# Kernel optimization log

Measured on AMD Instinct MI355X. Metric: run time of the kernel, lower is better.

The kernel has to match this reference:

```python
import jax, jax.numpy as jnp
import numpy as np

B, N = 4, 1024
D1, D2 = 512, 512
C = 512          # out_c = outdim_self[2] = ln_dim
H = 8            # cross_num_heads
DH = C // H      # head dim
LAYERS = 3       # cross_layer
LN_EPS = 1e-5


def _layer_norm(x, gamma, beta):
    mu = jnp.mean(x, axis=-1, keepdims=True)
    var = jnp.mean(jnp.square(x - mu), axis=-1, keepdims=True)
    return (x - mu) * jax.lax.rsqrt(var + LN_EPS) * gamma + beta


def setup_inputs() -> dict:
    key = jax.random.key(0)
    ks = jax.random.split(key, 5)
    s1, s2, sv = 1.0 / np.sqrt(D1), 1.0 / np.sqrt(D2), 1.0 / np.sqrt(D1 + D2)
    return {
        "x1": jax.random.normal(ks[0], (B, N, D1), jnp.float32),
        "x2": jax.random.normal(ks[1], (B, N, D2), jnp.float32),
        "Wq": jax.random.uniform(ks[2], (C, D1), jnp.float32, -s1, s1),
        "Wk": jax.random.uniform(ks[3], (C, D2), jnp.float32, -s2, s2),
        "Wv": jax.random.uniform(ks[4], (C, D1 + D2), jnp.float32, -sv, sv),
        "ln_gamma": jnp.ones((C,), jnp.float32),
        "ln_beta": jnp.zeros((C,), jnp.float32),
    }


def reference(x1, x2, Wq, Wk, Wv, ln_gamma, ln_beta):
    x = jnp.concatenate((x1, x2), axis=2)                      # [B,N,D1+D2]
    scale = x1.shape[-1] ** (-0.5)                             # uses x1 feature dim
    # [B,N,C] -> [B,H,N,DH]
    to_heads = lambda t: t.reshape(B, N, H, DH).transpose(0, 2, 1, 3)
    Q = to_heads(jnp.einsum('bnd,cd->bnc', x1, Wq))
    K = to_heads(jnp.einsum('bnd,cd->bnc', x2, Wk))
    V = to_heads(jnp.einsum('bnd,cd->bnc', x, Wv))

    output = None
    for _ in range(LAYERS):
        attn = jnp.einsum('bhnd,bhmd->bhnm', Q, K) * scale     # [B,H,N,N]
        mask = attn != 0
        attn = jnp.where(mask, attn, -1e20)
        attn = jax.nn.softmax(attn, axis=-1)
        attn = attn * mask
        V1 = jnp.einsum('bhnm,bhmd->bhnd', attn, V)            # [B,H,N,DH]
        V1 = V1.transpose(0, 2, 1, 3).reshape(B, N, C)
        Vr = V.transpose(0, 2, 1, 3).reshape(B, N, C)
        output = _layer_norm(V1 + Vr, ln_gamma, ln_beta)       # [B,N,C]
        V = to_heads(output)
    return output
```

## Files before the change

### kernel.cpp

```cpp
#include <hip/hip_runtime.h>


#define LOG2E 1.44269504088896f

using f32x4   = __attribute__((ext_vector_type(4))) float;
using short8  = __attribute__((ext_vector_type(8))) short;
using ushort8 = __attribute__((ext_vector_type(8))) unsigned short;
using ushort4v= __attribute__((ext_vector_type(4))) unsigned short;
using uchar8  = __attribute__((ext_vector_type(8))) unsigned char;
using uchar4v = __attribute__((ext_vector_type(4))) unsigned char;
using uchar16 = __attribute__((ext_vector_type(16))) unsigned char;

__device__ inline unsigned short f2bf(float f) {
  unsigned u = __builtin_bit_cast(unsigned, f);
  u += 0x7fffu + ((u >> 16) & 1u);
  return (unsigned short)(u >> 16);
}
__device__ inline float bf2f(unsigned short h) {
  unsigned u = (unsigned)h << 16;
  return __builtin_bit_cast(float, u);
}

__device__ inline unsigned char f2e4m3_fast(float f) {
  unsigned u = __builtin_bit_cast(unsigned, f);
  unsigned sign = (u >> 24) & 0x80u;
  unsigned a = u & 0x7fffffffu;
  unsigned v = a + (0x7ffffu + ((a >> 20) & 1u));
  unsigned m = (v >> 20) - 960u;
  m = (m > 126u) ? 126u : m;
  m = (a < 0x3c000000u) ? 0u : m;
  return (unsigned char)(sign | m);
}

__device__ inline f32x4 mfma_bf16(short8 a, short8 b, f32x4 c) {
  return __builtin_amdgcn_mfma_f32_16x16x32_bf16(a, b, c, 0, 0, 0);
}

__device__ inline void gload_lds16(const void* g, void* l) {
  __builtin_amdgcn_global_load_lds(
      (const __attribute__((address_space(1))) unsigned int*)g,
      (__attribute__((address_space(3))) unsigned int*)l, 16, 0, 0);
}

__device__ inline int swz(int row, int byte_in_row) {
  return row * 128 + (byte_in_row ^ ((row & 7) << 4));
}

__global__ __launch_bounds__(256) void k_convert_all(
    const float* __restrict__ x1, const float* __restrict__ x2,
    const float* __restrict__ Wq, const float* __restrict__ Wk,
    const float* __restrict__ Wv,
    unsigned short* __restrict__ xb, unsigned short* __restrict__ Wqb,
    unsigned short* __restrict__ Wkb, unsigned short* __restrict__ Wvb) {
  int i = blockIdx.x * 256 + threadIdx.x;
  const float* src;
  unsigned short* dst;
  if (i < 524288) {
    int e0 = i * 8, m = e0 >> 10, d = e0 & 1023;
    src = (d < 512) ? (x1 + (size_t)m * 512 + d)
                    : (x2 + (size_t)m * 512 + (d - 512));
    dst = xb + (size_t)e0;
  } else if (i < 557056) {
    int j = (i - 524288) * 8;
    src = Wq + j; dst = Wqb + j;
  } else if (i < 589824) {
    int j = (i - 557056) * 8;
    src = Wk + j; dst = Wkb + j;
  } else {
    int j = (i - 589824) * 8;
    src = Wv + j; dst = Wvb + j;
  }
  float4 a = ((const float4*)src)[0];
  float4 b = ((const float4*)src)[1];
  ushort8 o;
  o[0] = f2bf(a.x); o[1] = f2bf(a.y); o[2] = f2bf(a.z); o[3] = f2bf(a.w);
  o[4] = f2bf(b.x); o[5] = f2bf(b.y); o[6] = f2bf(b.z); o[7] = f2bf(b.w);
  *(ushort8*)dst = o;
}

__global__ __launch_bounds__(256) void k_proj(
    const unsigned short* __restrict__ xb,
    const unsigned short* __restrict__ Wqb,
    const unsigned short* __restrict__ Wkb,
    const unsigned short* __restrict__ Wvb,
    unsigned short* __restrict__ Qb, unsigned short* __restrict__ Kb,
    float* __restrict__ Vf, unsigned char* __restrict__ VtF8, int writeVt) {
  __shared__ __align__(16) unsigned short Atile[128 * 64];
  __shared__ __align__(16) unsigned short Btile[128 * 64];

  const int id  = blockIdx.x;
  const int z   = id % 3;
  const int rem = id / 3;
  const int c0  = (rem & 3) * 128;
  const int m0  = (rem >> 2) * 128;

  const int K    = (z == 2) ? 1024 : 512;
  const int aoff = (z == 1) ? 512 : 0;
  const unsigned short* W = (z == 0) ? Wqb : (z == 1) ? Wkb : Wvb;

  const int t  = threadIdx.x;
  const int w  = t >> 6, l = t & 63;
  const int lr = l & 15, ls = l >> 4;
  const int wr = w >> 1, wc = w & 1;

  const int srow  = l >> 3;
  const int scol8 = (l & 7) * 8;

  f32x4 acc[4][4] = {};

  for (int k0 = 0; k0 < K; k0 += 64) {
#pragma unroll
    for (int j = 0; j < 4; ++j) {
      int ch  = w * 4 + j;
      int row = ch * 8 + srow;
      gload_lds16(xb + (size_t)(m0 + row) * 1024 + aoff + k0 + scol8,
                  Atile + ch * 512);
      gload_lds16(W + (size_t)(c0 + row) * K + k0 + scol8,
                  Btile + ch * 512);
    }
    __syncthreads();
#pragma unroll
    for (int ks = 0; ks < 2; ++ks) {
      short8 af[4], bf[4];
#pragma unroll
      for (int mf = 0; mf < 4; ++mf)
        af[mf] = *(const short8*)(Atile + (wr * 64 + mf * 16 + lr) * 64 +
                                  ks * 32 + ls * 8);
#pragma unroll
      for (int nf = 0; nf < 4; ++nf)
        bf[nf] = *(const short8*)(Btile + (wc * 64 + nf * 16 + lr) * 64 +
                                  ks * 32 + ls * 8);
#pragma unroll
      for (int mf = 0; mf < 4; ++mf)
#pragma unroll
        for (int nf = 0; nf < 4; ++nf)
          acc[mf][nf] = mfma_bf16(af[mf], bf[nf], acc[mf][nf]);
    }
    __syncthreads();
  }

#pragma unroll
  for (int mf = 0; mf < 4; ++mf)
#pragma unroll
    for (int nf = 0; nf < 4; ++nf) {
      int m = m0 + wr * 64 + mf * 16 + ls * 4;
      int c = c0 + wc * 64 + nf * 16 + lr;
      if (z == 2) {
#pragma unroll
        for (int r = 0; r < 4; ++r)
          Vf[(size_t)(m + r) * 512 + c] = acc[mf][nf][r];
        if (writeVt) {
          int b = m >> 10, n = m & 1023, h = c >> 6, dh = c & 63;
          uchar4v o;
#pragma unroll
          for (int r = 0; r < 4; ++r) o[r] = f2e4m3_fast(acc[mf][nf][r]);
          char* dst = (char*)VtF8 +
                      ((size_t)((b * 8 + h) * 64 + dh)) * 1024 + (n & ~127) +
                      ((n & 127) ^ ((dh & 7) << 4));
          *(uchar4v*)dst = o;
        }
      } else {
#pragma unroll
        for (int r = 0; r < 4; ++r) {
          int mm = m + r;
          int b = mm >> 10, n = mm & 1023, h = c >> 6, dh = c & 63;
          size_t idx = ((size_t)(b * 8 + h) * 1024 + n) * 64 + dh;
          (z == 0 ? Qb : Kb)[idx] = f2bf(acc[mf][nf][r]);
        }
      }
    }
}

__global__ __launch_bounds__(256) void k_transpose_v(
    const float* __restrict__ Vf, void* __restrict__ Vt) {
  __shared__ unsigned short tile[64 * 66];
  const int bh = blockIdx.y;
  const int b = bh >> 3, h = bh & 7;
  const int n0 = blockIdx.x * 64;
  const int t = threadIdx.x;
  {
    int n = t >> 2, dh0 = (t & 3) * 16;
    const float* src = Vf + ((size_t)b * 1024 + n0 + n) * 512 + h * 64 + dh0;
    unsigned short* dst = tile + n * 66 + dh0;
#pragma unroll
    for (int j = 0; j < 16; j += 4) {
      float4 v = *(const float4*)(src + j);
      dst[j + 0] = f2bf(v.x); dst[j + 1] = f2bf(v.y);
      dst[j + 2] = f2bf(v.z); dst[j + 3] = f2bf(v.w);
    }
  }
  __syncthreads();
#pragma unroll
  for (int it = 0; it < 2; ++it) {
    int dh = (t >> 3) + it * 32, n8 = (t & 7) * 8;
    ushort8 o;
#pragma unroll
    for (int j = 0; j < 8; ++j) o[j] = tile[(n8 + j) * 66 + dh];
    char* dst = (char*)Vt + ((size_t)(bh * 64 + dh)) * 2048 + n0 * 2 +
                ((n8 * 2) ^ ((dh & 7) << 4));
    *(ushort8*)dst = o;
  }
}

__global__ __launch_bounds__(256) void k_scores(
    const unsigned short* __restrict__ Qb,
    const unsigned short* __restrict__ Kb,
    unsigned char* __restrict__ Pmat, float* __restrict__ lsum_g) {
  __shared__ char lds[2 * 8192 + 4 * 16 * 80];
  char* kbuf0 = lds;
  char* kbuf1 = lds + 8192;
  const int id  = blockIdx.x;
  const int lid = (id & 7) * 256 + (id >> 3);
  const int bh  = lid >> 6;
  const int q0  = ((lid >> 2) & 15) * 64;
  const int kq  = lid & 3;
  const int t = threadIdx.x;
  const int w = t >> 6, l = t & 63, lr = l & 15, ls = l >> 4;
  char* pbuf = lds + 16384 + w * (16 * 80);

  const float sclog2e = 0.0637587160f;

  short8 qa[2];
  {
    const unsigned short* Qg =
        Qb + ((size_t)bh * 1024 + q0 + w * 16 + lr) * 64 + ls * 8;
    qa[0] = *(const short8*)(Qg);
    qa[1] = *(const short8*)(Qg + 32);
  }

  const unsigned short* Kg = Kb + (size_t)bh * 1024 * 64 + kq * 256 * 64;
  unsigned char* Pg = Pmat + (size_t)bh * 1024 * 1024;

  float lacc[4] = {0.f, 0.f, 0.f, 0.f};

  const int srow = t >> 3, sc8 = (t & 7) * 8;
  int4 kreg[2];
  kreg[0] = *(const int4*)(Kg + (size_t)(srow)*64 + sc8);
  kreg[1] = *(const int4*)(Kg + (size_t)(srow + 32) * 64 + sc8);
  {
    char* kb = kbuf0;
    *(int4*)(kb + swz(srow, sc8 * 2)) = kreg[0];
    *(int4*)(kb + swz(srow + 32, sc8 * 2)) = kreg[1];
  }

  for (int kc = 0; kc < 4; ++kc) {
    __syncthreads();
    char* kb  = (kc & 1) ? kbuf1 : kbuf0;
    char* kbn = (kc & 1) ? kbuf0 : kbuf1;
    if (kc < 3) {
      kreg[0] = *(const int4*)(Kg + (size_t)((kc + 1) * 64 + srow) * 64 + sc8);
      kreg[1] = *(const int4*)(Kg + (size_t)((kc + 1) * 64 + srow + 32) * 64 + sc8);
    }

    f32x4 s[4] = {};
#pragma unroll
    for (int kk = 0; kk < 2; ++kk) {
#pragma unroll
      for (int nt = 0; nt < 4; ++nt) {
        short8 bk = *(const short8*)(kb + swz(nt * 16 + lr, kk * 64 + ls * 16));
        s[nt] = mfma_bf16(qa[kk], bk, s[nt]);
      }
    }

#pragma unroll
    for (int nt = 0; nt < 4; ++nt)
#pragma unroll
      for (int r = 0; r < 4; ++r) {
        float sv = s[nt][r];
        float pv = (sv == 0.f) ? 0.f : __builtin_amdgcn_exp2f(sv * sclog2e);
        lacc[r] += pv;
        pbuf[(ls * 4 + r) * 80 + nt * 16 + lr] = (char)f2e4m3_fast(pv);
      }

    int gkc = kq * 4 + kc;
    {
      int prow = l >> 2, pchk = l & 3;
      uchar16 pv16 = *(const uchar16*)(pbuf + prow * 80 + pchk * 16);
      int n = q0 + w * 16 + prow;
      *(uchar16*)(Pg + (size_t)n * 1024 + (gkc >> 1) * 128 +
                  (((gkc & 1) * 64 + pchk * 16) ^ ((n & 7) << 4))) = pv16;
    }

    if (kc < 3) {
      *(int4*)(kbn + swz(srow, sc8 * 2)) = kreg[0];
      *(int4*)(kbn + swz(srow + 32, sc8 * 2)) = kreg[1];
    }
  }

#pragma unroll
  for (int r = 0; r < 4; ++r) {
#pragma unroll
    for (int off = 1; off < 16; off <<= 1)
      lacc[r] += __shfl_xor(lacc[r], off, 64);
  }
  if (lr == 0) {
#pragma unroll
    for (int r = 0; r < 4; ++r)
      lsum_g[kq * 32768 + (size_t)bh * 1024 + q0 + w * 16 + ls * 4 + r] =
          lacc[r];
  }
}

__global__ __launch_bounds__(256) void k_pv(
    const unsigned char* __restrict__ Pmat,
    const unsigned char* __restrict__ Vt,
    const float* __restrict__ lsum_g, unsigned short* __restrict__ V1a,
    unsigned short* __restrict__ V1b) {
  __shared__ __align__(16) char Ab[2][8192];
  __shared__ __align__(16) char Bb[2][8192];
  const int id  = blockIdx.x;
  const int lid = (id & 7) * 128 + (id >> 3);
  const int head = lid >> 5;
  const int n0   = ((lid >> 1) & 15) * 64;
  const int mh   = lid & 1;
  const int t = threadIdx.x;
  const int w = t >> 6, l = t & 63, lr = l & 15, ls = l >> 4;

  const char* Pg = (const char*)(Pmat + (size_t)head * 1024 * 1024) +
                   (size_t)n0 * 1024 + mh * 512;
  const char* Vg = (const char*)(Vt + (size_t)head * 64 * 1024) + mh * 512;

  const int srow = w * 16 + (l >> 3);
  const int sc16 = (l & 7) * 16;

  f32x4 acc[4] = {};

  auto STAGE = [&](int buf, int kc) {
#pragma unroll
    for (int j = 0; j < 2; ++j) {
      int row = srow + j * 8;
      gload_lds16(Pg + (size_t)row * 1024 + kc * 128 + sc16,
                  &Ab[buf][w * 2048 + j * 1024]);
      gload_lds16(Vg + (size_t)row * 1024 + kc * 128 + sc16,
                  &Bb[buf][w * 2048 + j * 1024]);
    }
  };

  STAGE(0, 0);
  __syncthreads();
  int cur = 0;
  for (int kc = 0; kc < 4; ++kc) {
    if (kc < 3) STAGE(cur ^ 1, kc + 1);
#pragma unroll
    for (int ks = 0; ks < 4; ++ks) {
      long af = *(const long*)(&Ab[cur][swz(w * 16 + lr, ks * 32 + ls * 8)]);
#pragma unroll
      for (int nf = 0; nf < 4; ++nf) {
        long bf8 = *(const long*)(&Bb[cur][swz(nf * 16 + lr, ks * 32 + ls * 8)]);
        acc[nf] = __builtin_amdgcn_mfma_f32_16x16x32_fp8_fp8(af, bf8, acc[nf],
                                                             0, 0, 0);
      }
    }
    __syncthreads();
    cur ^= 1;
  }

  unsigned short* V1 = mh ? V1b : V1a;
  const int b = head >> 3, h = head & 7;
#pragma unroll
  for (int r = 0; r < 4; ++r) {
    int n = n0 + w * 16 + ls * 4 + r;
    size_t li = (size_t)head * 1024 + n;
    float lv = lsum_g[li] + lsum_g[32768 + li] + lsum_g[65536 + li] +
               lsum_g[98304 + li];
    float rinv = (lv > 0.f) ? 1.f / lv : 0.f;
#pragma unroll
    for (int nf = 0; nf < 4; ++nf)
      V1[((size_t)b * 1024 + n) * 512 + h * 64 + nf * 16 + lr] =
          f2bf(acc[nf][r] * rinv);
  }
}

__global__ __launch_bounds__(256) void k_ln_t(
    const unsigned short* __restrict__ V1a,
    const unsigned short* __restrict__ V1b,
    const float* __restrict__ Vf_in,
    const float* __restrict__ gamma, const float* __restrict__ beta,
    float* __restrict__ Vf_out, void* __restrict__ Vt, int mode) {
  __shared__ unsigned short tile[4 * 520];
  const int blk = blockIdx.x;
  const int b  = blk >> 8;
  const int n0 = (blk & 255) * 4;
  const int t = threadIdx.x;
  const int row = t >> 6;
  const int l = t & 63;
  const int c0 = l * 8;
  const size_t base = ((size_t)b * 1024 + n0 + row) * 512 + c0;

  float x[8];
  float s = 0.f, sq = 0.f;
  {
    ushort8 a0 = *(const ushort8*)(V1a + base);
    ushort8 a1 = *(const ushort8*)(V1b + base);
    float4 v0 = *(const float4*)(Vf_in + base);
    float4 v1 = *(const float4*)(Vf_in + base + 4);
#pragma unroll
    for (int j = 0; j < 8; ++j) {
      float vf = (j < 4) ? ((const float*)&v0)[j] : ((const float*)&v1)[j - 4];
      float y = bf2f(a0[j]) + bf2f(a1[j]) + vf;
      x[j] = y;
      s += y;
      sq += y * y;
    }
  }
#pragma unroll
  for (int off = 1; off < 64; off <<= 1) {
    s  += __shfl_xor(s, off, 64);
    sq += __shfl_xor(sq, off, 64);
  }
  float mu   = s * (1.f / 512.f);
  float var  = sq * (1.f / 512.f) - mu * mu;
  float rstd = rsqrtf(var + 1e-5f);

  unsigned short* trow = tile + row * 520 + c0;
#pragma unroll
  for (int j = 0; j < 8; j += 4) {
    float4 g = *(const float4*)(gamma + c0 + j);
    float4 bb = *(const float4*)(beta + c0 + j);
    float4 y;
    y.x = (x[j + 0] - mu) * rstd * g.x + bb.x;
    y.y = (x[j + 1] - mu) * rstd * g.y + bb.y;
    y.z = (x[j + 2] - mu) * rstd * g.z + bb.z;
    y.w = (x[j + 3] - mu) * rstd * g.w + bb.w;
    *(float4*)(Vf_out + base + j) = y;
    if (mode != 2) {
      trow[j + 0] = f2bf(y.x); trow[j + 1] = f2bf(y.y);
      trow[j + 2] = f2bf(y.z); trow[j + 3] = f2bf(y.w);
    }
  }
  if (mode == 2) return;
  __syncthreads();

#pragma unroll
  for (int it = 0; it < 2; ++it) {
    int d = t + it * 256;
    int h = d >> 6, dh = d & 63;
    int sw = (dh & 7) << 4;
    if (mode == 0) {
      ushort4v o;
#pragma unroll
      for (int j = 0; j < 4; ++j) o[j] = tile[j * 520 + d];
      int byte0 = n0 * 2;
      char* dst = (char*)Vt + ((size_t)((b * 8 + h) * 64 + dh)) * 2048 +
                  (byte0 & ~127) + ((byte0 & 127) ^ sw);
      *(ushort4v*)dst = o;
    } else {
      uchar4v o;
#pragma unroll
      for (int j = 0; j < 4; ++j) o[j] = f2e4m3_fast(bf2f(tile[j * 520 + d]));
      char* dst = (char*)Vt + ((size_t)((b * 8 + h) * 64 + dh)) * 1024 +
                  (n0 & ~127) + ((n0 & 127) ^ sw);
      *(uchar4v*)dst = o;
    }
  }
}

__global__ __launch_bounds__(256) void k_attn(
    const unsigned short* __restrict__ Qb,
    const unsigned short* __restrict__ Kb,
    const unsigned short* __restrict__ Vt,
    unsigned short* __restrict__ V1) {
  __shared__ char lds[8192 + 8192 + 4 * 16 * 144];
  char* kbuf = lds;
  char* vbuf = lds + 8192;
  const int bh = blockIdx.y;
  const int q0 = blockIdx.x * 64;
  const int t = threadIdx.x;
  const int w = t >> 6, l = t & 63, lr = l & 15, ls = l >> 4;
  char* pbuf = lds + 16384 + w * (16 * 144);

  const float scale = 0.044194173824159216f;

  short8 qa[2];
  {
    const unsigned short* Qg =
        Qb + ((size_t)bh * 1024 + q0 + w * 16 + lr) * 64 + ls * 8;
    qa[0] = *(const short8*)(Qg);
    qa[1] = *(const short8*)(Qg + 32);
  }

  f32x4 O[4] = {};
  float mrow[4], lrow[4];
#pragma unroll
  for (int r = 0; r < 4; ++r) { mrow[r] = -INFINITY; lrow[r] = 0.f; }

  const unsigned short* Kg = Kb + (size_t)bh * 1024 * 64;
  const char* Vg = (const char*)(Vt + (size_t)bh * 64 * 1024);

  for (int kc = 0; kc < 16; ++kc) {
    {
      int row = t >> 3;
      int c8  = (t & 7) * 8;
#pragma unroll
      for (int it = 0; it < 2; ++it) {
        int rr = row + it * 32;
        int4 kv = *(const int4*)(Kg + (size_t)(kc * 64 + rr) * 64 + c8);
        *(int4*)(kbuf + swz(rr, c8 * 2)) = kv;
        int swv = (rr & 7) << 4;
        int4 vv = *(const int4*)(Vg + (size_t)rr * 2048 + kc * 128 +
                                 ((c8 * 2) ^ swv));
        *(int4*)(vbuf + swz(rr, c8 * 2)) = vv;
      }
    }
    __syncthreads();

    f32x4 s[4] = {};
#pragma unroll
    for (int kk = 0; kk < 2; ++kk) {
#pragma unroll
      for (int nt = 0; nt < 4; ++nt) {
        short8 bk = *(const short8*)(kbuf + swz(nt * 16 + lr, kk * 64 + ls * 16));
        s[nt] = mfma_bf16(qa[kk], bk, s[nt]);
      }
    }

    float p[4][4];
    float cmax[4];
#pragma unroll
    for (int r = 0; r < 4; ++r) cmax[r] = -INFINITY;
#pragma unroll
    for (int nt = 0; nt < 4; ++nt)
#pragma unroll
      for (int r = 0; r < 4; ++r) {
        float sv = s[nt][r];
        p[nt][r] = (sv == 0.f) ? -INFINITY : sv * scale;
        cmax[r] = fmaxf(cmax[r], p[nt][r]);
      }
#pragma unroll
    for (int r = 0; r < 4; ++r)
#pragma unroll
      for (int off = 1; off < 16; off <<= 1)
        cmax[r] = fmaxf(cmax[r], __shfl_xor(cmax[r], off, 64));

    float alpha[4];
#pragma unroll
    for (int r = 0; r < 4; ++r) {
      float mnew = fmaxf(mrow[r], cmax[r]);
      alpha[r] = (mnew == -INFINITY) ? 1.f : exp2f((mrow[r] - mnew) * LOG2E);
      mrow[r] = mnew;
    }
    float lsum[4] = {0.f, 0.f, 0.f, 0.f};
#pragma unroll
    for (int nt = 0; nt < 4; ++nt)
#pragma unroll
      for (int r = 0; r < 4; ++r) {
        float pv = (p[nt][r] == -INFINITY)
                       ? 0.f
                       : exp2f((p[nt][r] - mrow[r]) * LOG2E);
        p[nt][r] = pv;
        lsum[r] += pv;
      }
#pragma unroll
    for (int r = 0; r < 4; ++r) {
#pragma unroll
      for (int off = 1; off < 16; off <<= 1)
        lsum[r] += __shfl_xor(lsum[r], off, 64);
      lrow[r] = lrow[r] * alpha[r] + lsum[r];
    }
#pragma unroll
    for (int dt = 0; dt < 4; ++dt)
#pragma unroll
      for (int r = 0; r < 4; ++r) O[dt][r] *= alpha[r];

#pragma unroll
    for (int nt = 0; nt < 4; ++nt)
#pragma unroll
      for (int r = 0; r < 4; ++r)
        *(unsigned short*)(pbuf + (ls * 4 + r) * 144 + (nt * 16 + lr) * 2) =
            f2bf(p[nt][r]);

#pragma unroll
    for (int kk = 0; kk < 2; ++kk) {
      short8 pa = *(const short8*)(pbuf + lr * 144 + kk * 64 + ls * 16);
#pragma unroll
      for (int dt = 0; dt < 4; ++dt) {
        short8 bv = *(const short8*)(vbuf + swz(dt * 16 + lr, kk * 64 + ls * 16));
        O[dt] = mfma_bf16(pa, bv, O[dt]);
      }
    }
    __syncthreads();
  }

  float rinv[4];
#pragma unroll
  for (int r = 0; r < 4; ++r) rinv[r] = (lrow[r] > 0.f) ? 1.f / lrow[r] : 0.f;
  const int b = bh >> 3, h = bh & 7;
#pragma unroll
  for (int dt = 0; dt < 4; ++dt)
#pragma unroll
    for (int r = 0; r < 4; ++r) {
      int n = q0 + w * 16 + ls * 4 + r;
      int c = h * 64 + dt * 16 + lr;
      V1[((size_t)b * 1024 + n) * 512 + c] = f2bf(O[dt][r] * rinv[r]);
    }
}

extern "C" void kernel_launch(void* const* d_in, const int* in_sizes, int n_in,
                              void* d_out, int out_size, void* d_ws,
                              size_t ws_size, hipStream_t stream) {
  const float* x1    = (const float*)d_in[0];
  const float* x2    = (const float*)d_in[1];
  const float* Wq    = (const float*)d_in[2];
  const float* Wk    = (const float*)d_in[3];
  const float* Wv    = (const float*)d_in[4];
  const float* gamma = (const float*)d_in[5];
  const float* beta  = (const float*)d_in[6];
  float* out = (float*)d_out;
  char* ws = (char*)d_ws;

  const size_t MB = 1u << 20;
  unsigned short* xb  = (unsigned short*)(ws);
  unsigned short* Wqb = (unsigned short*)(ws + 8 * MB);
  unsigned short* Wkb = (unsigned short*)(ws + 8 * MB + 512 * 1024);
  unsigned short* Wvb = (unsigned short*)(ws + 9 * MB);
  unsigned short* Qb  = (unsigned short*)(ws + 10 * MB);
  unsigned short* Kb  = (unsigned short*)(ws + 14 * MB);
  void*           Vt  = (void*)(ws + 18 * MB);
  float*          Vf  = (float*)(ws + 22 * MB);
  unsigned short* V1a = (unsigned short*)(ws + 30 * MB);
  float*          lsm = (float*)(ws + 38 * MB);
  unsigned char*  Pm  = (unsigned char*)(ws + 39 * MB);
  unsigned short* V1b = (unsigned short*)(ws);

  const bool bigws = ws_size >= (size_t)71 * MB;

  k_convert_all<<<2560, 256, 0, stream>>>(x1, x2, Wq, Wk, Wv, xb, Wqb, Wkb,
                                          Wvb);
  k_proj<<<384, 256, 0, stream>>>(xb, Wqb, Wkb, Wvb, Qb, Kb, Vf,
                                  (unsigned char*)Vt, bigws ? 1 : 0);

  if (bigws) {
    k_scores<<<2048, 256, 0, stream>>>(Qb, Kb, Pm, lsm);
    for (int layer = 0; layer < 3; ++layer) {
      k_pv<<<1024, 256, 0, stream>>>(Pm, (const unsigned char*)Vt, lsm, V1a,
                                     V1b);
      if (layer < 2)
        k_ln_t<<<1024, 256, 0, stream>>>(V1a, V1b, Vf, gamma, beta, Vf, Vt, 1);
      else
        k_ln_t<<<1024, 256, 0, stream>>>(V1a, V1b, Vf, gamma, beta, out, Vt, 2);
    }
  } else {
    hipMemsetAsync(V1b, 0, 4 * MB, stream);
    k_transpose_v<<<dim3(16, 32), 256, 0, stream>>>(Vf, Vt);
    for (int layer = 0; layer < 3; ++layer) {
      k_attn<<<dim3(16, 32), 256, 0, stream>>>(Qb, Kb,
                                               (const unsigned short*)Vt, V1a);
      if (layer < 2)
        k_ln_t<<<1024, 256, 0, stream>>>(V1a, V1b, Vf, gamma, beta, Vf, Vt, 0);
      else
        k_ln_t<<<1024, 256, 0, stream>>>(V1a, V1b, Vf, gamma, beta, out, Vt, 2);
    }
  }
}
```

Before: 118.4 us.

## Store residual V in bf16 and halve projection tile rows to double grid

The residual V buffer carried between layers changes from fp32 to bf16. The projection, transpose and layer-norm kernels now read and write half the bytes for it. The projection GEMM tile also shrinks from 128 to 64 rows, doubling the block count from 384 to 768 so the GPU's compute units are better filled, at the cost of less operand reuse per block. Rounding the residual to bf16 adds error that carries across the three layers.

```diff
diff --git a/kernel.cpp b/kernel.cpp
--- a/kernel.cpp
+++ b/kernel.cpp
@@ -84,15 +84,16 @@
     const unsigned short* __restrict__ Wkb,
     const unsigned short* __restrict__ Wvb,
     unsigned short* __restrict__ Qb, unsigned short* __restrict__ Kb,
-    float* __restrict__ Vf, unsigned char* __restrict__ VtF8, int writeVt) {
-  __shared__ __align__(16) unsigned short Atile[128 * 64];
+    unsigned short* __restrict__ Vf, unsigned char* __restrict__ VtF8,
+    int writeVt) {
+  __shared__ __align__(16) unsigned short Atile[64 * 64];
   __shared__ __align__(16) unsigned short Btile[128 * 64];
 
   const int id  = blockIdx.x;
   const int z   = id % 3;
   const int rem = id / 3;
   const int c0  = (rem & 3) * 128;
-  const int m0  = (rem >> 2) * 128;
+  const int m0  = (rem >> 2) * 64;
 
   const int K    = (z == 2) ? 1024 : 512;
   const int aoff = (z == 1) ? 512 : 0;
@@ -101,39 +102,43 @@
   const int t  = threadIdx.x;
   const int w  = t >> 6, l = t & 63;
   const int lr = l & 15, ls = l >> 4;
-  const int wr = w >> 1, wc = w & 1;
 
   const int srow  = l >> 3;
   const int scol8 = (l & 7) * 8;
 
-  f32x4 acc[4][4] = {};
+  f32x4 acc[4][2] = {};
 
   for (int k0 = 0; k0 < K; k0 += 64) {
+#pragma unroll
+    for (int j = 0; j < 2; ++j) {
+      int ch  = w * 2 + j;
+      int row = ch * 8 + srow;
+      gload_lds16(xb + (size_t)(m0 + row) * 1024 + aoff + k0 + scol8,
+                  Atile + ch * 512);
+    }
 #pragma unroll
     for (int j = 0; j < 4; ++j) {
       int ch  = w * 4 + j;
       int row = ch * 8 + srow;
-      gload_lds16(xb + (size_t)(m0 + row) * 1024 + aoff + k0 + scol8,
-                  Atile + ch * 512);
       gload_lds16(W + (size_t)(c0 + row) * K + k0 + scol8,
                   Btile + ch * 512);
     }
     __syncthreads();
 #pragma unroll
     for (int ks = 0; ks < 2; ++ks) {
-      short8 af[4], bf[4];
+      short8 af[4], bf[2];
 #pragma unroll
       for (int mf = 0; mf < 4; ++mf)
-        af[mf] = *(const short8*)(Atile + (wr * 64 + mf * 16 + lr) * 64 +
+        af[mf] = *(const short8*)(Atile + (mf * 16 + lr) * 64 + ks * 32 +
+                                  ls * 8);
+#pragma unroll
+      for (int nf = 0; nf < 2; ++nf)
+        bf[nf] = *(const short8*)(Btile + (w * 32 + nf * 16 + lr) * 64 +
                                   ks * 32 + ls * 8);
 #pragma unroll
-      for (int nf = 0; nf < 4; ++nf)
-        bf[nf] = *(const short8*)(Btile + (wc * 64 + nf * 16 + lr) * 64 +
-                                  ks * 32 + ls * 8);
-#pragma unroll
       for (int mf = 0; mf < 4; ++mf)
 #pragma unroll
-        for (int nf = 0; nf < 4; ++nf)
+        for (int nf = 0; nf < 2; ++nf)
           acc[mf][nf] = mfma_bf16(af[mf], bf[nf], acc[mf][nf]);
     }
     __syncthreads();
@@ -142,13 +147,13 @@
 #pragma unroll
   for (int mf = 0; mf < 4; ++mf)
 #pragma unroll
-    for (int nf = 0; nf < 4; ++nf) {
-      int m = m0 + wr * 64 + mf * 16 + ls * 4;
-      int c = c0 + wc * 64 + nf * 16 + lr;
+    for (int nf = 0; nf < 2; ++nf) {
+      int m = m0 + mf * 16 + ls * 4;
+      int c = c0 + w * 32 + nf * 16 + lr;
       if (z == 2) {
 #pragma unroll
         for (int r = 0; r < 4; ++r)
-          Vf[(size_t)(m + r) * 512 + c] = acc[mf][nf][r];
+          Vf[(size_t)(m + r) * 512 + c] = f2bf(acc[mf][nf][r]);
         if (writeVt) {
           int b = m >> 10, n = m & 1023, h = c >> 6, dh = c & 63;
           uchar4v o;
@@ -172,7 +177,7 @@
 }
 
 __global__ __launch_bounds__(256) void k_transpose_v(
-    const float* __restrict__ Vf, void* __restrict__ Vt) {
+    const unsigned short* __restrict__ Vf, void* __restrict__ Vt) {
   __shared__ unsigned short tile[64 * 66];
   const int bh = blockIdx.y;
   const int b = bh >> 3, h = bh & 7;
@@ -180,14 +185,11 @@
   const int t = threadIdx.x;
   {
     int n = t >> 2, dh0 = (t & 3) * 16;
-    const float* src = Vf + ((size_t)b * 1024 + n0 + n) * 512 + h * 64 + dh0;
+    const unsigned short* src =
+        Vf + ((size_t)b * 1024 + n0 + n) * 512 + h * 64 + dh0;
     unsigned short* dst = tile + n * 66 + dh0;
 #pragma unroll
-    for (int j = 0; j < 16; j += 4) {
-      float4 v = *(const float4*)(src + j);
-      dst[j + 0] = f2bf(v.x); dst[j + 1] = f2bf(v.y);
-      dst[j + 2] = f2bf(v.z); dst[j + 3] = f2bf(v.w);
-    }
+    for (int j = 0; j < 16; j += 8) *(ushort8*)(dst + j) = *(const ushort8*)(src + j);
   }
   __syncthreads();
 #pragma unroll
@@ -374,9 +376,10 @@
 __global__ __launch_bounds__(256) void k_ln_t(
     const unsigned short* __restrict__ V1a,
     const unsigned short* __restrict__ V1b,
-    const float* __restrict__ Vf_in,
+    const unsigned short* __restrict__ Vf_in,
     const float* __restrict__ gamma, const float* __restrict__ beta,
-    float* __restrict__ Vf_out, void* __restrict__ Vt, int mode) {
+    unsigned short* __restrict__ VfO, float* __restrict__ outF,
+    void* __restrict__ Vt, int mode) {
   __shared__ unsigned short tile[4 * 520];
   const int blk = blockIdx.x;
   const int b  = blk >> 8;
@@ -392,12 +395,10 @@
   {
     ushort8 a0 = *(const ushort8*)(V1a + base);
     ushort8 a1 = *(const ushort8*)(V1b + base);
-    float4 v0 = *(const float4*)(Vf_in + base);
-    float4 v1 = *(const float4*)(Vf_in + base + 4);
+    ushort8 vv = *(const ushort8*)(Vf_in + base);
 #pragma unroll
     for (int j = 0; j < 8; ++j) {
-      float vf = (j < 4) ? ((const float*)&v0)[j] : ((const float*)&v1)[j - 4];
-      float y = bf2f(a0[j]) + bf2f(a1[j]) + vf;
+      float y = bf2f(a0[j]) + bf2f(a1[j]) + bf2f(vv[j]);
       x[j] = y;
       s += y;
       sq += y * y;
@@ -422,10 +423,15 @@
     y.y = (x[j + 1] - mu) * rstd * g.y + bb.y;
     y.z = (x[j + 2] - mu) * rstd * g.z + bb.z;
     y.w = (x[j + 3] - mu) * rstd * g.w + bb.w;
-    *(float4*)(Vf_out + base + j) = y;
-    if (mode != 2) {
-      trow[j + 0] = f2bf(y.x); trow[j + 1] = f2bf(y.y);
-      trow[j + 2] = f2bf(y.z); trow[j + 3] = f2bf(y.w);
+    if (mode == 2) {
+      *(float4*)(outF + base + j) = y;
+    } else {
+      ushort4v yb;
+      yb[0] = f2bf(y.x); yb[1] = f2bf(y.y);
+      yb[2] = f2bf(y.z); yb[3] = f2bf(y.w);
+      *(ushort4v*)(VfO + base + j) = yb;
+      trow[j + 0] = yb[0]; trow[j + 1] = yb[1];
+      trow[j + 2] = yb[2]; trow[j + 3] = yb[3];
     }
   }
   if (mode == 2) return;
@@ -616,7 +622,7 @@
   unsigned short* Qb  = (unsigned short*)(ws + 10 * MB);
   unsigned short* Kb  = (unsigned short*)(ws + 14 * MB);
   void*           Vt  = (void*)(ws + 18 * MB);
-  float*          Vf  = (float*)(ws + 22 * MB);
+  unsigned short* Vf  = (unsigned short*)(ws + 22 * MB);
   unsigned short* V1a = (unsigned short*)(ws + 30 * MB);
   float*          lsm = (float*)(ws + 38 * MB);
   unsigned char*  Pm  = (unsigned char*)(ws + 39 * MB);
@@ -626,7 +632,7 @@
 
   k_convert_all<<<2560, 256, 0, stream>>>(x1, x2, Wq, Wk, Wv, xb, Wqb, Wkb,
                                           Wvb);
-  k_proj<<<384, 256, 0, stream>>>(xb, Wqb, Wkb, Wvb, Qb, Kb, Vf,
+  k_proj<<<768, 256, 0, stream>>>(xb, Wqb, Wkb, Wvb, Qb, Kb, Vf,
                                   (unsigned char*)Vt, bigws ? 1 : 0);
 
   if (bigws) {
@@ -635,9 +641,11 @@
       k_pv<<<1024, 256, 0, stream>>>(Pm, (const unsigned char*)Vt, lsm, V1a,
                                      V1b);
       if (layer < 2)
-        k_ln_t<<<1024, 256, 0, stream>>>(V1a, V1b, Vf, gamma, beta, Vf, Vt, 1);
+        k_ln_t<<<1024, 256, 0, stream>>>(V1a, V1b, Vf, gamma, beta, Vf, out,
+                                         Vt, 1);
       else
-        k_ln_t<<<1024, 256, 0, stream>>>(V1a, V1b, Vf, gamma, beta, out, Vt, 2);
+        k_ln_t<<<1024, 256, 0, stream>>>(V1a, V1b, Vf, gamma, beta, Vf, out,
+                                         Vt, 2);
     }
   } else {
     hipMemsetAsync(V1b, 0, 4 * MB, stream);
@@ -646,9 +654,11 @@
       k_attn<<<dim3(16, 32), 256, 0, stream>>>(Qb, Kb,
                                                (const unsigned short*)Vt, V1a);
       if (layer < 2)
-        k_ln_t<<<1024, 256, 0, stream>>>(V1a, V1b, Vf, gamma, beta, Vf, Vt, 0);
+        k_ln_t<<<1024, 256, 0, stream>>>(V1a, V1b, Vf, gamma, beta, Vf, out,
+                                         Vt, 0);
       else
-        k_ln_t<<<1024, 256, 0, stream>>>(V1a, V1b, Vf, gamma, beta, out, Vt, 2);
-    }
-  }
-}
+        k_ln_t<<<1024, 256, 0, stream>>>(V1a, V1b, Vf, gamma, beta, Vf, out,
+                                         Vt, 2);
+    }
+  }
+}
```

After: 111.5 us, median of 2. -5.8%, faster.
